# Performance work log

Hardware: AMD Instinct MI355X
Metric: run time of the kernel (lower is better)

The kernel has to match this reference:

```python
import jax, jax.numpy as jnp
import numpy as np

NHEAD = 4
HEAD_DIM = 64  # att_features per head = atten_feats // nhead


def setup_inputs() -> dict:
    key = jax.random.key(0)
    ks = jax.random.split(key, 8)
    N, D = 8192, 256
    s = 1.0 / np.sqrt(D)
    return {
        "x": jax.random.normal(ks[0], (N, D), dtype=jnp.float32),
        "edge": jax.random.randint(ks[1], (N, N), 0, 2, dtype=jnp.int32),
        "Wq": jax.random.normal(ks[2], (D, D), dtype=jnp.float32) * s,
        "bq": jax.random.normal(ks[3], (D,), dtype=jnp.float32) * 0.01,
        "Wk": jax.random.normal(ks[4], (D, D), dtype=jnp.float32) * s,
        "bk": jax.random.normal(ks[5], (D,), dtype=jnp.float32) * 0.01,
        "Wv": jax.random.normal(ks[6], (D, D), dtype=jnp.float32) * s,
        "bv": jax.random.normal(ks[7], (D,), dtype=jnp.float32) * 0.01,
    }


def _split_heads(t):
    # (N, H*d) -> (H, N, d)
    N = t.shape[0]
    return t.reshape(N, NHEAD, HEAD_DIM).transpose(1, 0, 2)


def reference(x, edge, Wq, bq, Wk, bk, Wv, bv):
    q = _split_heads(x @ Wq + bq)  # (H, N, d)
    k = _split_heads(x @ Wk + bk)
    v = _split_heads(x @ Wv + bv)
    # additive graph mask: 0 where edge.T == 1, -10000 where edge.T == 0
    mask = (edge.T.astype(jnp.float32) - 1.0) * 10000.0  # (N, N)
    scores = jnp.einsum("hnd,hmd->hnm", q, k) / np.sqrt(HEAD_DIM)
    scores = scores + mask[None, :, :]
    attn = jax.nn.softmax(scores, axis=-1)  # dropout is identity at eval
    ctx = jnp.einsum("hnm,hmd->hnd", attn, v)
    # (H, N, d) -> (N, H*d)
    return ctx.transpose(1, 0, 2).reshape(x.shape[0], NHEAD * HEAD_DIM)
```

## Files before the change

### kernel.cpp

```cpp
#include <hip/hip_runtime.h>
#include <stdint.h>

typedef unsigned short u16;
typedef unsigned int u32;
typedef unsigned long long u64;

typedef __attribute__((ext_vector_type(8))) __bf16 bf16x8;
typedef __attribute__((ext_vector_type(4))) float f32x4;

#define NROW 8192
#define DMODEL 256
#define HD 64
#define LDT 72

__device__ __forceinline__ u16 f2bf(float f) {
    u32 u = __builtin_bit_cast(u32, f);
    u += 0x7FFFu + ((u >> 16) & 1u);
    return (u16)(u >> 16);
}
__device__ __forceinline__ bf16x8 ldb8(const u16* p) {
    uint4 v = *(const uint4*)p;
    return __builtin_bit_cast(bf16x8, v);
}
__device__ __forceinline__ f32x4 mfma16(bf16x8 a, bf16x8 b, f32x4 c) {
    return __builtin_amdgcn_mfma_f32_16x16x32_bf16(a, b, c, 0, 0, 0);
}

__global__ __launch_bounds__(256) void k_prep(
    const float* __restrict__ x,
    const float* __restrict__ Wq, const float* __restrict__ Wk,
    const float* __restrict__ Wv,
    u16* __restrict__ xb, u16* __restrict__ Wt) {
    const int t = threadIdx.x;
    if (blockIdx.x < 1024) {
        size_t idx = (size_t)blockIdx.x * 2048 + t * 8;
        f32x4 a = *(const f32x4*)&x[idx];
        f32x4 b = *(const f32x4*)&x[idx + 4];
        uint4 o;
        o.x = (u32)f2bf(a[0]) | ((u32)f2bf(a[1]) << 16);
        o.y = (u32)f2bf(a[2]) | ((u32)f2bf(a[3]) << 16);
        o.z = (u32)f2bf(b[0]) | ((u32)f2bf(b[1]) << 16);
        o.w = (u32)f2bf(b[2]) | ((u32)f2bf(b[3]) << 16);
        *(uint4*)&xb[idx] = o;
        return;
    }
    __shared__ __align__(16) u16 lw[64 * LDT];
    int wb = blockIdx.x - 1024;
    int mat = wb >> 4, tile = wb & 15;
    int k0 = (tile >> 2) * 64, n0 = (tile & 3) * 64;
    const float* W = (mat == 0) ? Wq : ((mat == 1) ? Wk : Wv);
    #pragma unroll
    for (int i = 0; i < 4; ++i) {
        int c = t + 256 * i;
        int k = c >> 4, c4 = c & 15;
        f32x4 w4 = *(const f32x4*)&W[(size_t)(k0 + k) * DMODEL + n0 + c4 * 4];
        uint2 pk;
        pk.x = (u32)f2bf(w4[0]) | ((u32)f2bf(w4[1]) << 16);
        pk.y = (u32)f2bf(w4[2]) | ((u32)f2bf(w4[3]) << 16);
        *(uint2*)&lw[k * LDT + c4 * 4] = pk;
    }
    __syncthreads();
    #pragma unroll
    for (int i = 0; i < 2; ++i) {
        int c = t + 256 * i;
        int n = c >> 3, k8 = c & 7;
        union { uint4 u; u16 s[8]; } pk;
        #pragma unroll
        for (int j = 0; j < 8; ++j) pk.s[j] = lw[(k8 * 8 + j) * LDT + n];
        *(uint4*)&Wt[(size_t)mat * 65536 + (size_t)(n0 + n) * DMODEL + k0 + k8 * 8] = pk.u;
    }
}

__global__ __launch_bounds__(256, 4) void k_bitmask(const int* __restrict__ edge,
                                                    u64* __restrict__ bits) {
    const int lane = threadIdx.x & 63;
    const int wv = threadIdx.x >> 6;
    const u32 m = blockIdx.x * 4u + (u32)wv;
    const size_t rbase = (size_t)m * NROW;
    for (int cc = 0; cc < 32; cc += 2) {
        int v[8];
        #pragma unroll
        for (int j = 0; j < 4; ++j) v[j]     = edge[rbase + cc * 256 + j * 64 + lane];
        #pragma unroll
        for (int j = 0; j < 4; ++j) v[4 + j] = edge[rbase + cc * 256 + 256 + j * 64 + lane];
        u64 b[8];
        #pragma unroll
        for (int j = 0; j < 8; ++j) b[j] = __ballot(v[j] != 0);
        if (lane == 0) {
            #pragma unroll
            for (int j = 0; j < 8; ++j) bits[(size_t)(cc * 4 + j) * NROW + m] = b[j];
        }
    }
}

__global__ __launch_bounds__(256, 3) void k_qkv(
    const u16* __restrict__ xb, const u16* __restrict__ Wt,
    const float* __restrict__ bq, const float* __restrict__ bk,
    const float* __restrict__ bv,
    u16* __restrict__ Qo, u16* __restrict__ Ko, u16* __restrict__ Vt) {
    __shared__ __align__(16) u16 ax[128 * LDT];
    __shared__ __align__(16) u16 wt[64 * LDT];
    const int t = threadIdx.x;
    const int lane = t & 63, wv = t >> 6;
    const int q4 = lane >> 4, l15 = lane & 15;
    const int wr = wv >> 1, wc = wv & 1;
    const int row0 = blockIdx.x * 128;
    const int mat = blockIdx.y >> 2;
    const int c0 = (blockIdx.y & 3) * 64;
    const u16* Wm = Wt + (size_t)mat * 65536;
    const float* bias = (mat == 0) ? bq : ((mat == 1) ? bk : bv);

    f32x4 acc[8];
    #pragma unroll
    for (int i = 0; i < 8; ++i) acc[i] = {0.f, 0.f, 0.f, 0.f};

    for (int kk = 0; kk < DMODEL; kk += 64) {
        #pragma unroll
        for (int i = 0; i < 4; ++i) {
            int c = t + 256 * i;
            int row = c >> 3, c8 = c & 7;
            *(uint4*)&ax[row * LDT + c8 * 8] =
                *(const uint4*)&xb[(size_t)(row0 + row) * DMODEL + kk + c8 * 8];
        }
        #pragma unroll
        for (int i = 0; i < 2; ++i) {
            int c = t + 256 * i;
            int n = c >> 3, c8 = c & 7;
            *(uint4*)&wt[n * LDT + c8 * 8] =
                *(const uint4*)&Wm[(size_t)(c0 + n) * DMODEL + kk + c8 * 8];
        }
        __syncthreads();
        #pragma unroll
        for (int ks = 0; ks < 2; ++ks) {
            bf16x8 xf[4], wf[2];
            #pragma unroll
            for (int it = 0; it < 4; ++it)
                xf[it] = ldb8(&ax[(wr * 64 + it * 16 + l15) * LDT + ks * 32 + q4 * 8]);
            #pragma unroll
            for (int jt = 0; jt < 2; ++jt)
                wf[jt] = ldb8(&wt[(wc * 32 + jt * 16 + l15) * LDT + ks * 32 + q4 * 8]);
            if (mat < 2) {
                #pragma unroll
                for (int it = 0; it < 4; ++it)
                    #pragma unroll
                    for (int jt = 0; jt < 2; ++jt)
                        acc[it * 2 + jt] = mfma16(xf[it], wf[jt], acc[it * 2 + jt]);
            } else {
                #pragma unroll
                for (int jt = 0; jt < 2; ++jt)
                    #pragma unroll
                    for (int it = 0; it < 4; ++it)
                        acc[jt * 4 + it] = mfma16(wf[jt], xf[it], acc[jt * 4 + it]);
            }
        }
        __syncthreads();
    }

    if (mat < 2) {
        u16* out = (mat == 0) ? Qo : Ko;
        const float scale = (mat == 0) ? 0.18033688f : 1.0f;
        #pragma unroll
        for (int jt = 0; jt < 2; ++jt) {
            int col = c0 + wc * 32 + jt * 16 + l15;
            float bcol = bias[col];
            #pragma unroll
            for (int it = 0; it < 4; ++it) {
                int rowb = row0 + wr * 64 + it * 16 + q4 * 4;
                f32x4 a = acc[it * 2 + jt];
                #pragma unroll
                for (int r = 0; r < 4; ++r)
                    out[(size_t)(rowb + r) * DMODEL + col] = f2bf((a[r] + bcol) * scale);
            }
        }
    } else {
        #pragma unroll
        for (int jt = 0; jt < 2; ++jt) {
            #pragma unroll
            for (int r = 0; r < 4; ++r) {
                int drow = c0 + wc * 32 + jt * 16 + q4 * 4 + r;
                float bd = bias[drow];
                #pragma unroll
                for (int it = 0; it < 4; ++it) {
                    int col = row0 + wr * 64 + it * 16 + l15;
                    Vt[(size_t)drow * NROW + col] = f2bf(acc[jt * 4 + it][r] + bd);
                }
            }
        }
    }
}

__global__ __launch_bounds__(256, 2) void k_attn(
    const u16* __restrict__ Q, const u16* __restrict__ K,
    const u16* __restrict__ Vt, const u64* __restrict__ bits,
    float* __restrict__ out) {
    __shared__ __align__(16) u16 sK[2][64 * LDT];
    __shared__ __align__(16) u16 sV[2][64 * LDT];
    __shared__ __align__(16) u16 sP[4][16 * LDT];
    __shared__ __align__(16) u32 sB[2][2][64];

    const int t = threadIdx.x;
    const int lane = t & 63, w = t >> 6;
    const int q4 = lane >> 4, l15 = lane & 15;
    const int bid = blockIdx.x;
    const int h = (bid >> 1) & 3;
    const int qt = ((bid >> 3) << 1) | (bid & 1);
    const int n0 = qt * 64;
    const int half = w >> 1;
    const u32 shift = (u32)((w & 1) * 16 + l15);
    const int sr = t >> 3, sc8 = (t & 7) * 8;

    bf16x8 qf[2];
    #pragma unroll
    for (int ks = 0; ks < 2; ++ks)
        qf[ks] = ldb8(&Q[(size_t)(n0 + w * 16 + l15) * DMODEL + h * HD + ks * 32 + q4 * 8]);

    uint4 onesu = {0x3F803F80u, 0x3F803F80u, 0x3F803F80u, 0x3F803F80u};
    const bf16x8 ones = __builtin_bit_cast(bf16x8, onesu);

    f32x4 o[4], lacc;
    lacc = {0.f, 0.f, 0.f, 0.f};
    #pragma unroll
    for (int dt = 0; dt < 4; ++dt) o[dt] = {0.f, 0.f, 0.f, 0.f};

    uint4 rk0, rk1, rv0, rv1; uint2 rb;
    {
        rk0 = *(const uint4*)&K[(size_t)(0 + sr) * DMODEL + h * HD + sc8];
        rk1 = *(const uint4*)&K[(size_t)(32 + sr) * DMODEL + h * HD + sc8];
        rv0 = *(const uint4*)&Vt[(size_t)(h * HD + sr) * NROW + 0 + sc8];
        rv1 = *(const uint4*)&Vt[(size_t)(h * HD + 32 + sr) * NROW + 0 + sc8];
        if (t < 64) rb = *(const uint2*)&bits[(size_t)qt * NROW + 0 + t];
        *(uint4*)&sK[0][sr * LDT + sc8] = rk0;
        *(uint4*)&sK[0][(32 + sr) * LDT + sc8] = rk1;
        *(uint4*)&sV[0][sr * LDT + sc8] = rv0;
        *(uint4*)&sV[0][(32 + sr) * LDT + sc8] = rv1;
        if (t < 64) { sB[0][0][t] = rb.x; sB[0][1][t] = rb.y; }
    }

    for (int kt = 0; kt < 128; ++kt) {
        __syncthreads();
        const int buf = kt & 1;
        if (kt < 127) {
            int m0 = (kt + 1) * 64;
            rk0 = *(const uint4*)&K[(size_t)(m0 + sr) * DMODEL + h * HD + sc8];
            rk1 = *(const uint4*)&K[(size_t)(m0 + 32 + sr) * DMODEL + h * HD + sc8];
            rv0 = *(const uint4*)&Vt[(size_t)(h * HD + sr) * NROW + m0 + sc8];
            rv1 = *(const uint4*)&Vt[(size_t)(h * HD + 32 + sr) * NROW + m0 + sc8];
            if (t < 64) rb = *(const uint2*)&bits[(size_t)qt * NROW + m0 + t];
        }

        f32x4 s[4];
        #pragma unroll
        for (int tj = 0; tj < 4; ++tj) s[tj] = {0.f, 0.f, 0.f, 0.f};
        #pragma unroll
        for (int ks = 0; ks < 2; ++ks) {
            bf16x8 kb[4];
            #pragma unroll
            for (int tj = 0; tj < 4; ++tj)
                kb[tj] = ldb8(&sK[buf][(tj * 16 + l15) * LDT + ks * 32 + q4 * 8]);
            #pragma unroll
            for (int tj = 0; tj < 4; ++tj)
                s[tj] = mfma16(kb[tj], qf[ks], s[tj]);
        }

        #pragma unroll
        for (int tj = 0; tj < 4; ++tj) {
            uint4 bw = *(const uint4*)&sB[buf][half][tj * 16 + q4 * 4];
            u32 wd[4] = {bw.x, bw.y, bw.z, bw.w};
            u32 ub[4];
            #pragma unroll
            for (int r = 0; r < 4; ++r) {
                float sv = ((wd[r] >> shift) & 1u) ? s[tj][r] : -1e30f;
                ub[r] = __builtin_bit_cast(u32, __builtin_amdgcn_exp2f(sv));
            }
            uint2 pk;
            pk.x = (ub[0] >> 16) | (ub[1] & 0xFFFF0000u);
            pk.y = (ub[2] >> 16) | (ub[3] & 0xFFFF0000u);
            *(uint2*)&sP[w][l15 * LDT + tj * 16 + q4 * 4] = pk;
        }
        asm volatile("s_waitcnt lgkmcnt(0)" ::: "memory");

        #pragma unroll
        for (int ks = 0; ks < 2; ++ks) {
            bf16x8 pf = ldb8(&sP[w][l15 * LDT + ks * 32 + q4 * 8]);
            bf16x8 vb[4];
            #pragma unroll
            for (int dt = 0; dt < 4; ++dt)
                vb[dt] = ldb8(&sV[buf][(dt * 16 + l15) * LDT + ks * 32 + q4 * 8]);
            #pragma unroll
            for (int dt = 0; dt < 4; ++dt)
                o[dt] = mfma16(pf, vb[dt], o[dt]);
            lacc = mfma16(pf, ones, lacc);
        }

        if (kt < 127) {
            const int nb = buf ^ 1;
            *(uint4*)&sK[nb][sr * LDT + sc8] = rk0;
            *(uint4*)&sK[nb][(32 + sr) * LDT + sc8] = rk1;
            *(uint4*)&sV[nb][sr * LDT + sc8] = rv0;
            *(uint4*)&sV[nb][(32 + sr) * LDT + sc8] = rv1;
            if (t < 64) { sB[nb][0][t] = rb.x; sB[nb][1][t] = rb.y; }
        }
    }

    #pragma unroll
    for (int r = 0; r < 4; ++r) {
        float inv = __builtin_amdgcn_rcpf(lacc[r] + 1e-30f);
        int n = n0 + w * 16 + q4 * 4 + r;
        #pragma unroll
        for (int dt = 0; dt < 4; ++dt)
            out[(size_t)n * DMODEL + h * HD + dt * 16 + l15] = o[dt][r] * inv;
    }
}

extern "C" void kernel_launch(void* const* d_in, const int* in_sizes, int n_in,
                              void* d_out, int out_size, void* d_ws, size_t ws_size,
                              hipStream_t stream) {
    const float* x  = (const float*)d_in[0];
    const int* edge = (const int*)d_in[1];
    const float* Wq = (const float*)d_in[2];
    const float* bq = (const float*)d_in[3];
    const float* Wk = (const float*)d_in[4];
    const float* bk = (const float*)d_in[5];
    const float* Wv = (const float*)d_in[6];
    const float* bv = (const float*)d_in[7];

    char* ws = (char*)d_ws;
    u64* bits = (u64*)ws;
    u16* Qo  = (u16*)(ws + (8u << 20));
    u16* Ko  = (u16*)(ws + (12u << 20));
    u16* Vt  = (u16*)(ws + (16u << 20));
    u16* xb  = (u16*)(ws + (20u << 20));
    u16* Wt  = (u16*)(ws + (24u << 20));
    float* out = (float*)d_out;

    hipLaunchKernelGGL(k_prep, dim3(1072), dim3(256), 0, stream, x, Wq, Wk, Wv, xb, Wt);
    hipLaunchKernelGGL(k_bitmask, dim3(2048), dim3(256), 0, stream, edge, bits);
    hipLaunchKernelGGL(k_qkv, dim3(64, 12), dim3(256), 0, stream,
                       xb, Wt, bq, bk, bv, Qo, Ko, Vt);
    hipLaunchKernelGGL(k_attn, dim3(512), dim3(256), 0, stream, Qo, Ko, Vt, bits, out);
}
```

Before: 543.9 us.

## Split attention keys across waves with 128-key tiles and cross-wave reduction

The attention kernel now has each wave handle all 64 query rows against its own 32-key slice of a 128-key tile, instead of each wave owning 16 query rows. Each K/V fragment read from LDS therefore feeds four MFMAs, and the key loop runs half as many iterations. Partial outputs and row sums are merged across waves through shared memory at the end. The bitmask kernel also loads 16 values per iteration instead of 8. The costs are more accumulator registers, single-buffered LDS with two barriers per iteration, and a serialized final reduction.

```diff
diff --git a/kernel.cpp b/kernel.cpp
--- a/kernel.cpp
+++ b/kernel.cpp
@@ -77,18 +77,16 @@
     const int wv = threadIdx.x >> 6;
     const u32 m = blockIdx.x * 4u + (u32)wv;
     const size_t rbase = (size_t)m * NROW;
-    for (int cc = 0; cc < 32; cc += 2) {
-        int v[8];
-        #pragma unroll
-        for (int j = 0; j < 4; ++j) v[j]     = edge[rbase + cc * 256 + j * 64 + lane];
-        #pragma unroll
-        for (int j = 0; j < 4; ++j) v[4 + j] = edge[rbase + cc * 256 + 256 + j * 64 + lane];
-        u64 b[8];
-        #pragma unroll
-        for (int j = 0; j < 8; ++j) b[j] = __ballot(v[j] != 0);
+    for (int cc = 0; cc < 32; cc += 4) {
+        int v[16];
+        #pragma unroll
+        for (int j = 0; j < 16; ++j) v[j] = edge[rbase + cc * 256 + j * 64 + lane];
+        u64 b[16];
+        #pragma unroll
+        for (int j = 0; j < 16; ++j) b[j] = __ballot(v[j] != 0);
         if (lane == 0) {
             #pragma unroll
-            for (int j = 0; j < 8; ++j) bits[(size_t)(cc * 4 + j) * NROW + m] = b[j];
+            for (int j = 0; j < 16; ++j) bits[(size_t)(cc * 4 + j) * NROW + m] = b[j];
         }
     }
 }
@@ -193,10 +191,10 @@
     const u16* __restrict__ Q, const u16* __restrict__ K,
     const u16* __restrict__ Vt, const u64* __restrict__ bits,
     float* __restrict__ out) {
-    __shared__ __align__(16) u16 sK[2][64 * LDT];
-    __shared__ __align__(16) u16 sV[2][64 * LDT];
-    __shared__ __align__(16) u16 sP[4][16 * LDT];
-    __shared__ __align__(16) u32 sB[2][2][64];
+    __shared__ __align__(16) u16 sK[128 * LDT];
+    __shared__ __align__(16) u16 sV[64 * 136];
+    __shared__ __align__(16) u16 sP[4][64 * 40];
+    __shared__ __align__(16) u32 sB[2][128];
 
     const int t = threadIdx.x;
     const int lane = t & 63, w = t >> 6;
@@ -205,110 +203,136 @@
     const int h = (bid >> 1) & 3;
     const int qt = ((bid >> 3) << 1) | (bid & 1);
     const int n0 = qt * 64;
-    const int half = w >> 1;
-    const u32 shift = (u32)((w & 1) * 16 + l15);
-    const int sr = t >> 3, sc8 = (t & 7) * 8;
-
-    bf16x8 qf[2];
-    #pragma unroll
-    for (int ks = 0; ks < 2; ++ks)
-        qf[ks] = ldb8(&Q[(size_t)(n0 + w * 16 + l15) * DMODEL + h * HD + ks * 32 + q4 * 8]);
+    u16* sPw = &sP[w][0];
+
+    bf16x8 qf[4][2];
+    #pragma unroll
+    for (int nt = 0; nt < 4; ++nt)
+        #pragma unroll
+        for (int ks = 0; ks < 2; ++ks)
+            qf[nt][ks] = ldb8(&Q[(size_t)(n0 + nt * 16 + l15) * DMODEL + h * HD + ks * 32 + q4 * 8]);
 
     uint4 onesu = {0x3F803F80u, 0x3F803F80u, 0x3F803F80u, 0x3F803F80u};
     const bf16x8 ones = __builtin_bit_cast(bf16x8, onesu);
 
-    f32x4 o[4], lacc;
-    lacc = {0.f, 0.f, 0.f, 0.f};
-    #pragma unroll
-    for (int dt = 0; dt < 4; ++dt) o[dt] = {0.f, 0.f, 0.f, 0.f};
-
-    uint4 rk0, rk1, rv0, rv1; uint2 rb;
-    {
-        rk0 = *(const uint4*)&K[(size_t)(0 + sr) * DMODEL + h * HD + sc8];
-        rk1 = *(const uint4*)&K[(size_t)(32 + sr) * DMODEL + h * HD + sc8];
-        rv0 = *(const uint4*)&Vt[(size_t)(h * HD + sr) * NROW + 0 + sc8];
-        rv1 = *(const uint4*)&Vt[(size_t)(h * HD + 32 + sr) * NROW + 0 + sc8];
-        if (t < 64) rb = *(const uint2*)&bits[(size_t)qt * NROW + 0 + t];
-        *(uint4*)&sK[0][sr * LDT + sc8] = rk0;
-        *(uint4*)&sK[0][(32 + sr) * LDT + sc8] = rk1;
-        *(uint4*)&sV[0][sr * LDT + sc8] = rv0;
-        *(uint4*)&sV[0][(32 + sr) * LDT + sc8] = rv1;
-        if (t < 64) { sB[0][0][t] = rb.x; sB[0][1][t] = rb.y; }
-    }
-
-    for (int kt = 0; kt < 128; ++kt) {
-        __syncthreads();
-        const int buf = kt & 1;
-        if (kt < 127) {
-            int m0 = (kt + 1) * 64;
-            rk0 = *(const uint4*)&K[(size_t)(m0 + sr) * DMODEL + h * HD + sc8];
-            rk1 = *(const uint4*)&K[(size_t)(m0 + 32 + sr) * DMODEL + h * HD + sc8];
-            rv0 = *(const uint4*)&Vt[(size_t)(h * HD + sr) * NROW + m0 + sc8];
-            rv1 = *(const uint4*)&Vt[(size_t)(h * HD + 32 + sr) * NROW + m0 + sc8];
-            if (t < 64) rb = *(const uint2*)&bits[(size_t)qt * NROW + m0 + t];
-        }
-
-        f32x4 s[4];
-        #pragma unroll
-        for (int tj = 0; tj < 4; ++tj) s[tj] = {0.f, 0.f, 0.f, 0.f};
-        #pragma unroll
-        for (int ks = 0; ks < 2; ++ks) {
-            bf16x8 kb[4];
-            #pragma unroll
-            for (int tj = 0; tj < 4; ++tj)
-                kb[tj] = ldb8(&sK[buf][(tj * 16 + l15) * LDT + ks * 32 + q4 * 8]);
-            #pragma unroll
-            for (int tj = 0; tj < 4; ++tj)
-                s[tj] = mfma16(kb[tj], qf[ks], s[tj]);
-        }
-
-        #pragma unroll
-        for (int tj = 0; tj < 4; ++tj) {
-            uint4 bw = *(const uint4*)&sB[buf][half][tj * 16 + q4 * 4];
-            u32 wd[4] = {bw.x, bw.y, bw.z, bw.w};
-            u32 ub[4];
-            #pragma unroll
-            for (int r = 0; r < 4; ++r) {
-                float sv = ((wd[r] >> shift) & 1u) ? s[tj][r] : -1e30f;
-                ub[r] = __builtin_bit_cast(u32, __builtin_amdgcn_exp2f(sv));
-            }
-            uint2 pk;
-            pk.x = (ub[0] >> 16) | (ub[1] & 0xFFFF0000u);
-            pk.y = (ub[2] >> 16) | (ub[3] & 0xFFFF0000u);
-            *(uint2*)&sP[w][l15 * LDT + tj * 16 + q4 * 4] = pk;
+    f32x4 o[4][4];
+    f32x4 lacc[4];
+    #pragma unroll
+    for (int nt = 0; nt < 4; ++nt) {
+        lacc[nt] = {0.f, 0.f, 0.f, 0.f};
+        #pragma unroll
+        for (int dt = 0; dt < 4; ++dt) o[dt][nt] = {0.f, 0.f, 0.f, 0.f};
+    }
+
+    const int krow = t >> 3, kc8 = (t & 7) * 8;
+    const int vrow = t >> 4, vc16 = (t & 15) * 8;
+
+    uint4 rk[4], rv[4]; uint2 rb;
+    #pragma unroll
+    for (int i = 0; i < 4; ++i) {
+        rk[i] = *(const uint4*)&K[(size_t)(i * 32 + krow) * DMODEL + h * HD + kc8];
+        rv[i] = *(const uint4*)&Vt[(size_t)(h * HD + i * 16 + vrow) * NROW + vc16];
+    }
+    if (t < 128) rb = *(const uint2*)&bits[(size_t)qt * NROW + t];
+
+    for (int kt = 0; kt < 64; ++kt) {
+        #pragma unroll
+        for (int i = 0; i < 4; ++i) {
+            *(uint4*)&sK[(i * 32 + krow) * LDT + kc8] = rk[i];
+            *(uint4*)&sV[(i * 16 + vrow) * 136 + vc16] = rv[i];
+        }
+        if (t < 128) { sB[0][t] = rb.x; sB[1][t] = rb.y; }
+        __syncthreads();
+
+        if (kt < 63) {
+            int m0n = (kt + 1) * 128;
+            #pragma unroll
+            for (int i = 0; i < 4; ++i) {
+                rk[i] = *(const uint4*)&K[(size_t)(m0n + i * 32 + krow) * DMODEL + h * HD + kc8];
+                rv[i] = *(const uint4*)&Vt[(size_t)(h * HD + i * 16 + vrow) * NROW + m0n + vc16];
+            }
+            if (t < 128) rb = *(const uint2*)&bits[(size_t)qt * NROW + m0n + t];
+        }
+
+        f32x4 s[2][4];
+        #pragma unroll
+        for (int tjm = 0; tjm < 2; ++tjm) {
+            #pragma unroll
+            for (int nt = 0; nt < 4; ++nt) s[tjm][nt] = {0.f, 0.f, 0.f, 0.f};
+            #pragma unroll
+            for (int ks = 0; ks < 2; ++ks) {
+                bf16x8 kb = ldb8(&sK[(w * 32 + tjm * 16 + l15) * LDT + ks * 32 + q4 * 8]);
+                #pragma unroll
+                for (int nt = 0; nt < 4; ++nt)
+                    s[tjm][nt] = mfma16(kb, qf[nt][ks], s[tjm][nt]);
+            }
+        }
+
+        #pragma unroll
+        for (int tjm = 0; tjm < 2; ++tjm) {
+            #pragma unroll
+            for (int nt = 0; nt < 4; ++nt) {
+                uint4 bw = *(const uint4*)&sB[nt >> 1][w * 32 + tjm * 16 + q4 * 4];
+                u32 wd[4] = {bw.x, bw.y, bw.z, bw.w};
+                const u32 shift = (u32)((nt & 1) * 16 + l15);
+                u32 ub[4];
+                #pragma unroll
+                for (int r = 0; r < 4; ++r) {
+                    float sv = ((wd[r] >> shift) & 1u) ? s[tjm][nt][r] : -1e30f;
+                    ub[r] = __builtin_bit_cast(u32, __builtin_amdgcn_exp2f(sv));
+                }
+                uint2 pk;
+                pk.x = (ub[0] >> 16) | (ub[1] & 0xFFFF0000u);
+                pk.y = (ub[2] >> 16) | (ub[3] & 0xFFFF0000u);
+                *(uint2*)&sPw[(nt * 16 + l15) * 40 + tjm * 16 + q4 * 4] = pk;
+            }
         }
         asm volatile("s_waitcnt lgkmcnt(0)" ::: "memory");
 
-        #pragma unroll
-        for (int ks = 0; ks < 2; ++ks) {
-            bf16x8 pf = ldb8(&sP[w][l15 * LDT + ks * 32 + q4 * 8]);
-            bf16x8 vb[4];
-            #pragma unroll
-            for (int dt = 0; dt < 4; ++dt)
-                vb[dt] = ldb8(&sV[buf][(dt * 16 + l15) * LDT + ks * 32 + q4 * 8]);
-            #pragma unroll
-            for (int dt = 0; dt < 4; ++dt)
-                o[dt] = mfma16(pf, vb[dt], o[dt]);
-            lacc = mfma16(pf, ones, lacc);
-        }
-
-        if (kt < 127) {
-            const int nb = buf ^ 1;
-            *(uint4*)&sK[nb][sr * LDT + sc8] = rk0;
-            *(uint4*)&sK[nb][(32 + sr) * LDT + sc8] = rk1;
-            *(uint4*)&sV[nb][sr * LDT + sc8] = rv0;
-            *(uint4*)&sV[nb][(32 + sr) * LDT + sc8] = rv1;
-            if (t < 64) { sB[nb][0][t] = rb.x; sB[nb][1][t] = rb.y; }
-        }
-    }
-
-    #pragma unroll
-    for (int r = 0; r < 4; ++r) {
-        float inv = __builtin_amdgcn_rcpf(lacc[r] + 1e-30f);
-        int n = n0 + w * 16 + q4 * 4 + r;
-        #pragma unroll
-        for (int dt = 0; dt < 4; ++dt)
-            out[(size_t)n * DMODEL + h * HD + dt * 16 + l15] = o[dt][r] * inv;
+        bf16x8 pf[4];
+        #pragma unroll
+        for (int nt = 0; nt < 4; ++nt)
+            pf[nt] = ldb8(&sPw[(nt * 16 + l15) * 40 + q4 * 8]);
+        #pragma unroll
+        for (int dt = 0; dt < 4; ++dt) {
+            bf16x8 vb = ldb8(&sV[(dt * 16 + l15) * 136 + w * 32 + q4 * 8]);
+            #pragma unroll
+            for (int nt = 0; nt < 4; ++nt)
+                o[dt][nt] = mfma16(vb, pf[nt], o[dt][nt]);
+        }
+        #pragma unroll
+        for (int nt = 0; nt < 4; ++nt)
+            lacc[nt] = mfma16(ones, pf[nt], lacc[nt]);
+        __syncthreads();
+    }
+
+    float* S = (float*)sK;
+    #pragma unroll 1
+    for (int p = 0; p < 4; ++p) {
+        if (w == p) {
+            #pragma unroll
+            for (int nt = 0; nt < 4; ++nt) {
+                #pragma unroll
+                for (int dt = 0; dt < 4; ++dt) {
+                    f32x4* dst = (f32x4*)&S[(nt * 16 + l15) * 68 + dt * 16 + q4 * 4];
+                    *dst = (p == 0) ? o[dt][nt] : (*dst + o[dt][nt]);
+                }
+                if (q4 == 0) {
+                    float* lp = &S[64 * 68 + nt * 16 + l15];
+                    *lp = (p == 0) ? lacc[nt][0] : (*lp + lacc[nt][0]);
+                }
+            }
+        }
+        __syncthreads();
+    }
+    #pragma unroll
+    for (int j = 0; j < 4; ++j) {
+        int n = j * 16 + (t >> 4);
+        int d0 = (t & 15) * 4;
+        float inv = __builtin_amdgcn_rcpf(S[64 * 68 + n] + 1e-30f);
+        f32x4 v = *(f32x4*)&S[n * 68 + d0];
+        v = v * inv;
+        *(f32x4*)&out[(size_t)(n0 + n) * DMODEL + h * HD + d0] = v;
     }
 }
 
```

New measurement: 592.1 us. +8.9%, slower.

## Widen attention key tiles to 128, swizzle LDS, and vectorize bitmask packing

Applied to the files above, without the earlier changes.

The bitmask kernel now reads edge rows as int4, ballots four interleaved bit-planes, and stages them in shared memory so the packed bits are written with coalesced 16-byte stores. The attention kernel processes 128 keys per iteration with a single shared buffer and XOR-swizzled K/V/P layouts instead of padded rows, and indexes the bitmask through the new interleaved packing. The aim is fewer barriers per key, fewer LDS bank conflicts, and cheaper mask generation. In exchange, loads for the next tile are no longer double-buffered in LDS, each thread holds more prefetch registers, and the mask bit indexing becomes more intricate.

```diff
diff --git a/kernel.cpp b/kernel.cpp
--- a/kernel.cpp
+++ b/kernel.cpp
@@ -72,25 +72,41 @@
 }
 
 __global__ __launch_bounds__(256, 4) void k_bitmask(const int* __restrict__ edge,
-                                                    u64* __restrict__ bits) {
-    const int lane = threadIdx.x & 63;
-    const int wv = threadIdx.x >> 6;
-    const u32 m = blockIdx.x * 4u + (u32)wv;
-    const size_t rbase = (size_t)m * NROW;
-    for (int cc = 0; cc < 32; cc += 2) {
-        int v[8];
-        #pragma unroll
-        for (int j = 0; j < 4; ++j) v[j]     = edge[rbase + cc * 256 + j * 64 + lane];
-        #pragma unroll
-        for (int j = 0; j < 4; ++j) v[4 + j] = edge[rbase + cc * 256 + 256 + j * 64 + lane];
-        u64 b[8];
-        #pragma unroll
-        for (int j = 0; j < 8; ++j) b[j] = __ballot(v[j] != 0);
-        if (lane == 0) {
-            #pragma unroll
-            for (int j = 0; j < 8; ++j) bits[(size_t)(cc * 4 + j) * NROW + m] = b[j];
-        }
-    }
+                                                    u64* __restrict__ pbits) {
+    __shared__ u64 lb[128][8];
+    const int t = threadIdx.x;
+    const int lane = t & 63, w = t >> 6;
+    const u32 m8 = blockIdx.x * 8u;
+    #pragma unroll
+    for (int rr = 0; rr < 2; ++rr) {
+        const int mloc = w * 2 + rr;
+        const size_t base = (size_t)(m8 + mloc) * NROW;
+        for (int q0 = 0; q0 < 32; q0 += 4) {
+            int4 e[4];
+            #pragma unroll
+            for (int j = 0; j < 4; ++j)
+                e[j] = *(const int4*)&edge[base + (size_t)(q0 + j) * 256 + lane * 4];
+            #pragma unroll
+            for (int j = 0; j < 4; ++j) {
+                u64 b0 = __ballot(e[j].x != 0);
+                u64 b1 = __ballot(e[j].y != 0);
+                u64 b2 = __ballot(e[j].z != 0);
+                u64 b3 = __ballot(e[j].w != 0);
+                if (lane == 0) {
+                    lb[(q0 + j) * 4 + 0][mloc] = b0;
+                    lb[(q0 + j) * 4 + 1][mloc] = b1;
+                    lb[(q0 + j) * 4 + 2][mloc] = b2;
+                    lb[(q0 + j) * 4 + 3][mloc] = b3;
+                }
+            }
+        }
+    }
+    __syncthreads();
+    const int qc = t >> 1, r0 = (t & 1) * 4;
+    uint4 a = *(uint4*)&lb[qc][r0];
+    uint4 b = *(uint4*)&lb[qc][r0 + 2];
+    *(uint4*)&pbits[(size_t)qc * NROW + m8 + r0] = a;
+    *(uint4*)&pbits[(size_t)qc * NROW + m8 + r0 + 2] = b;
 }
 
 __global__ __launch_bounds__(256, 3) void k_qkv(
@@ -191,23 +207,28 @@
 
 __global__ __launch_bounds__(256, 2) void k_attn(
     const u16* __restrict__ Q, const u16* __restrict__ K,
-    const u16* __restrict__ Vt, const u64* __restrict__ bits,
+    const u16* __restrict__ Vt, const u64* __restrict__ pbits,
     float* __restrict__ out) {
-    __shared__ __align__(16) u16 sK[2][64 * LDT];
-    __shared__ __align__(16) u16 sV[2][64 * LDT];
-    __shared__ __align__(16) u16 sP[4][16 * LDT];
-    __shared__ __align__(16) u32 sB[2][2][64];
+    __shared__ __align__(16) u16 sK[128 * 64];
+    __shared__ __align__(16) u16 sV[64 * 128];
+    __shared__ __align__(16) u16 sP[4][2][16 * 64];
+    __shared__ __align__(16) u32 sB[4][132];
 
     const int t = threadIdx.x;
     const int lane = t & 63, w = t >> 6;
     const int q4 = lane >> 4, l15 = lane & 15;
+    const int l7 = l15 & 7;
     const int bid = blockIdx.x;
     const int h = (bid >> 1) & 3;
     const int qt = ((bid >> 3) << 1) | (bid & 1);
     const int n0 = qt * 64;
-    const int half = w >> 1;
-    const u32 shift = (u32)((w & 1) * 16 + l15);
-    const int sr = t >> 3, sc8 = (t & 7) * 8;
+    const int halfsel = (qt >> 1) & 1;
+    const int shiftv = ((((qt & 3) * 16 + w * 4) & 31)) + (l15 >> 2);
+    const int qbase = (qt >> 2) * 4;
+
+    const int krow = t >> 3, kc = t & 7;
+    const int vd = t >> 4, vc = t & 15;
+    const int bc = t >> 6, bm = t & 63;
 
     bf16x8 qf[2];
     #pragma unroll
@@ -222,83 +243,86 @@
     #pragma unroll
     for (int dt = 0; dt < 4; ++dt) o[dt] = {0.f, 0.f, 0.f, 0.f};
 
-    uint4 rk0, rk1, rv0, rv1; uint2 rb;
-    {
-        rk0 = *(const uint4*)&K[(size_t)(0 + sr) * DMODEL + h * HD + sc8];
-        rk1 = *(const uint4*)&K[(size_t)(32 + sr) * DMODEL + h * HD + sc8];
-        rv0 = *(const uint4*)&Vt[(size_t)(h * HD + sr) * NROW + 0 + sc8];
-        rv1 = *(const uint4*)&Vt[(size_t)(h * HD + 32 + sr) * NROW + 0 + sc8];
-        if (t < 64) rb = *(const uint2*)&bits[(size_t)qt * NROW + 0 + t];
-        *(uint4*)&sK[0][sr * LDT + sc8] = rk0;
-        *(uint4*)&sK[0][(32 + sr) * LDT + sc8] = rk1;
-        *(uint4*)&sV[0][sr * LDT + sc8] = rv0;
-        *(uint4*)&sV[0][(32 + sr) * LDT + sc8] = rv1;
-        if (t < 64) { sB[0][0][t] = rb.x; sB[0][1][t] = rb.y; }
-    }
-
-    for (int kt = 0; kt < 128; ++kt) {
+    const u32* pb32 = (const u32*)pbits;
+    uint4 rk[4], rv[4]; u32 rb[2];
+    #pragma unroll
+    for (int i = 0; i < 4; ++i) {
+        rk[i] = *(const uint4*)&K[(size_t)(i * 32 + krow) * DMODEL + h * HD + kc * 8];
+        rv[i] = *(const uint4*)&Vt[(size_t)(h * HD + i * 16 + vd) * NROW + vc * 8];
+    }
+    #pragma unroll
+    for (int i = 0; i < 2; ++i)
+        rb[i] = pb32[((size_t)(qbase + bc) * NROW + i * 64 + bm) * 2 + halfsel];
+
+    for (int kt = 0; kt < 64; ++kt) {
         __syncthreads();
-        const int buf = kt & 1;
-        if (kt < 127) {
-            int m0 = (kt + 1) * 64;
-            rk0 = *(const uint4*)&K[(size_t)(m0 + sr) * DMODEL + h * HD + sc8];
-            rk1 = *(const uint4*)&K[(size_t)(m0 + 32 + sr) * DMODEL + h * HD + sc8];
-            rv0 = *(const uint4*)&Vt[(size_t)(h * HD + sr) * NROW + m0 + sc8];
-            rv1 = *(const uint4*)&Vt[(size_t)(h * HD + 32 + sr) * NROW + m0 + sc8];
-            if (t < 64) rb = *(const uint2*)&bits[(size_t)qt * NROW + m0 + t];
-        }
-
-        f32x4 s[4];
-        #pragma unroll
-        for (int tj = 0; tj < 4; ++tj) s[tj] = {0.f, 0.f, 0.f, 0.f};
-        #pragma unroll
-        for (int ks = 0; ks < 2; ++ks) {
-            bf16x8 kb[4];
-            #pragma unroll
-            for (int tj = 0; tj < 4; ++tj)
-                kb[tj] = ldb8(&sK[buf][(tj * 16 + l15) * LDT + ks * 32 + q4 * 8]);
-            #pragma unroll
-            for (int tj = 0; tj < 4; ++tj)
-                s[tj] = mfma16(kb[tj], qf[ks], s[tj]);
-        }
-
-        #pragma unroll
-        for (int tj = 0; tj < 4; ++tj) {
-            uint4 bw = *(const uint4*)&sB[buf][half][tj * 16 + q4 * 4];
-            u32 wd[4] = {bw.x, bw.y, bw.z, bw.w};
-            u32 ub[4];
-            #pragma unroll
-            for (int r = 0; r < 4; ++r) {
-                float sv = ((wd[r] >> shift) & 1u) ? s[tj][r] : -1e30f;
-                ub[r] = __builtin_bit_cast(u32, __builtin_amdgcn_exp2f(sv));
-            }
-            uint2 pk;
-            pk.x = (ub[0] >> 16) | (ub[1] & 0xFFFF0000u);
-            pk.y = (ub[2] >> 16) | (ub[3] & 0xFFFF0000u);
-            *(uint2*)&sP[w][l15 * LDT + tj * 16 + q4 * 4] = pk;
+        #pragma unroll
+        for (int i = 0; i < 4; ++i) {
+            *(uint4*)&sK[(i * 32 + krow) * 64 + ((kc ^ (krow & 7)) * 8)] = rk[i];
+            *(uint4*)&sV[(i * 16 + vd) * 128 + ((vc ^ vd) * 8)] = rv[i];
+        }
+        sB[bc][bm] = rb[0];
+        sB[bc][64 + bm] = rb[1];
+        __syncthreads();
+
+        if (kt < 63) {
+            int m0n = (kt + 1) * 128;
+            #pragma unroll
+            for (int i = 0; i < 4; ++i) {
+                rk[i] = *(const uint4*)&K[(size_t)(m0n + i * 32 + krow) * DMODEL + h * HD + kc * 8];
+                rv[i] = *(const uint4*)&Vt[(size_t)(h * HD + i * 16 + vd) * NROW + m0n + vc * 8];
+            }
+            #pragma unroll
+            for (int i = 0; i < 2; ++i)
+                rb[i] = pb32[((size_t)(qbase + bc) * NROW + m0n + i * 64 + bm) * 2 + halfsel];
+        }
+
+        #pragma unroll
+        for (int half = 0; half < 2; ++half) {
+            f32x4 s[4];
+            #pragma unroll
+            for (int tj = 0; tj < 4; ++tj) s[tj] = {0.f, 0.f, 0.f, 0.f};
+            #pragma unroll
+            for (int ks = 0; ks < 2; ++ks) {
+                #pragma unroll
+                for (int tj = 0; tj < 4; ++tj) {
+                    bf16x8 kb = ldb8(&sK[(half * 64 + tj * 16 + l15) * 64 +
+                                         (((ks * 4 + q4) ^ l7) * 8)]);
+                    s[tj] = mfma16(kb, qf[ks], s[tj]);
+                }
+            }
+            #pragma unroll
+            for (int tj = 0; tj < 4; ++tj) {
+                uint4 bw = *(const uint4*)&sB[l15 & 3][half * 64 + tj * 16 + q4 * 4];
+                u32 wd[4] = {bw.x, bw.y, bw.z, bw.w};
+                u32 ub[4];
+                #pragma unroll
+                for (int r = 0; r < 4; ++r) {
+                    float sv = ((wd[r] >> shiftv) & 1u) ? s[tj][r] : -1e30f;
+                    ub[r] = __builtin_bit_cast(u32, __builtin_amdgcn_exp2f(sv));
+                }
+                uint2 pk;
+                pk.x = (ub[0] >> 16) | (ub[1] & 0xFFFF0000u);
+                pk.y = (ub[2] >> 16) | (ub[3] & 0xFFFF0000u);
+                *(uint2*)&sP[w][half][l15 * 64 +
+                                      (((tj * 2 + (q4 >> 1)) ^ l7) * 8) + (q4 & 1) * 4] = pk;
+            }
         }
         asm volatile("s_waitcnt lgkmcnt(0)" ::: "memory");
 
         #pragma unroll
-        for (int ks = 0; ks < 2; ++ks) {
-            bf16x8 pf = ldb8(&sP[w][l15 * LDT + ks * 32 + q4 * 8]);
-            bf16x8 vb[4];
-            #pragma unroll
-            for (int dt = 0; dt < 4; ++dt)
-                vb[dt] = ldb8(&sV[buf][(dt * 16 + l15) * LDT + ks * 32 + q4 * 8]);
-            #pragma unroll
-            for (int dt = 0; dt < 4; ++dt)
-                o[dt] = mfma16(pf, vb[dt], o[dt]);
-            lacc = mfma16(pf, ones, lacc);
-        }
-
-        if (kt < 127) {
-            const int nb = buf ^ 1;
-            *(uint4*)&sK[nb][sr * LDT + sc8] = rk0;
-            *(uint4*)&sK[nb][(32 + sr) * LDT + sc8] = rk1;
-            *(uint4*)&sV[nb][sr * LDT + sc8] = rv0;
-            *(uint4*)&sV[nb][(32 + sr) * LDT + sc8] = rv1;
-            if (t < 64) { sB[nb][0][t] = rb.x; sB[nb][1][t] = rb.y; }
+        for (int half = 0; half < 2; ++half) {
+            #pragma unroll
+            for (int ks = 0; ks < 2; ++ks) {
+                bf16x8 pf = ldb8(&sP[w][half][l15 * 64 + (((ks * 4 + q4) ^ l7) * 8)]);
+                #pragma unroll
+                for (int dt = 0; dt < 4; ++dt) {
+                    bf16x8 vb = ldb8(&sV[(dt * 16 + l15) * 128 +
+                                         (((half * 8 + ks * 4 + q4) ^ l15) * 8)]);
+                    o[dt] = mfma16(pf, vb, o[dt]);
+                }
+                lacc = mfma16(pf, ones, lacc);
+            }
         }
     }
 
@@ -325,7 +349,7 @@
     const float* bv = (const float*)d_in[7];
 
     char* ws = (char*)d_ws;
-    u64* bits = (u64*)ws;
+    u64* pbits = (u64*)ws;
     u16* Qo  = (u16*)(ws + (8u << 20));
     u16* Ko  = (u16*)(ws + (12u << 20));
     u16* Vt  = (u16*)(ws + (16u << 20));
@@ -334,8 +358,8 @@
     float* out = (float*)d_out;
 
     hipLaunchKernelGGL(k_prep, dim3(1072), dim3(256), 0, stream, x, Wq, Wk, Wv, xb, Wt);
-    hipLaunchKernelGGL(k_bitmask, dim3(2048), dim3(256), 0, stream, edge, bits);
+    hipLaunchKernelGGL(k_bitmask, dim3(1024), dim3(256), 0, stream, edge, pbits);
     hipLaunchKernelGGL(k_qkv, dim3(64, 12), dim3(256), 0, stream,
                        xb, Wt, bq, bk, bv, Qo, Ko, Vt);
-    hipLaunchKernelGGL(k_attn, dim3(512), dim3(256), 0, stream, Qo, Ko, Vt, bits, out);
-}
+    hipLaunchKernelGGL(k_attn, dim3(512), dim3(256), 0, stream, Qo, Ko, Vt, pbits, out);
+}
```

Result: slower. 749.8 us (+37.9%).
